# Kernel optimization log

Hardware: AMD Instinct MI355X
Metric: run time of the kernel (lower is better)

Reference implementation:

```python
import jax, jax.numpy as jnp
import numpy as np

B = 4096      # batch size per view (init arg bs)
D = 256       # embedding dim
TEMP = 0.5    # init arg temp
EPS = 1e-8    # torch CosineSimilarity eps


def setup_inputs() -> dict:
    key = jax.random.key(0)
    k1, k2 = jax.random.split(key)
    return {
        "emb1": jax.random.normal(k1, (B, D), dtype=jnp.float32),
        "emb2": jax.random.normal(k2, (B, D), dtype=jnp.float32),
    }


def reference(emb1, emb2):
    # z: (2B, D)
    z = jnp.concatenate([emb1, emb2], axis=0)
    n = 2 * B
    # Cosine similarity as normalize + GEMM (same math as broadcast CosineSimilarity):
    # sim[i,j] = (z_i . z_j) / max(||z_i||*||z_j||, eps), then / temp
    norms = jnp.linalg.norm(z, axis=-1)                       # (2B,)
    denom = jnp.maximum(norms[:, None] * norms[None, :], EPS)  # (2B,2B)
    sim = (z @ z.T) / denom / TEMP                             # (2B,2B)

    idx = jnp.arange(n)
    # positives: diag(sim, +B) then diag(sim, -B) == sim[i, (i+B) mod 2B]
    pos = sim[idx, (idx + B) % n]                              # (2B,)

    # logits row i = [pos_i, negatives_i] = all sim[i,:] except the diagonal.
    # cross-entropy with label 0: loss_i = -pos_i + logsumexp(row without diag)
    diag_mask = idx[:, None] == idx[None, :]
    sim_masked = jnp.where(diag_mask, -jnp.inf, sim)
    lse = jax.nn.logsumexp(sim_masked, axis=-1)                # (2B,)

    loss = jnp.sum(lse - pos) / n   # CrossEntropyLoss(reduction='sum') / 2B
    return loss
```

## Files before the change

kernel.cpp:

```cpp
#include <hip/hip_runtime.h>
#include <hip/hip_bf16.h>


constexpr int kN  = 8192;
constexpr int kD  = 256;
constexpr int kBH = 4096;
constexpr int kChunks  = 32;
constexpr int kColsPer = kN / kChunks;
constexpr float kInvTemp = 2.0f;
constexpr float kInvTempLog2e = 2.8853900817779268f;

typedef __attribute__((ext_vector_type(8))) short bf16x8;
typedef __attribute__((ext_vector_type(4))) float f32x4;

__device__ __forceinline__ unsigned short f2bf(float f) {
  union { float f; unsigned u; } x;
  x.f = f;
  unsigned u = x.u;
  return (unsigned short)((u + 0x7FFFu + ((u >> 16) & 1u)) >> 16);
}

__global__ void k_normalize(const float* __restrict__ e1,
                            const float* __restrict__ e2,
                            unsigned short* __restrict__ zn,
                            float* __restrict__ accum ) {
  if (blockIdx.x < 16) {
    float4 z4 = {0.f, 0.f, 0.f, 0.f};
    *reinterpret_cast<float4*>(accum + blockIdx.x * 1024 + threadIdx.x * 4) = z4;
  }
  const int wave = threadIdx.x >> 6;
  const int lane = threadIdx.x & 63;
  const int row  = blockIdx.x * 4 + wave;
  const float* src = (row < kBH) ? (e1 + (size_t)row * kD)
                                 : (e2 + (size_t)(row - kBH) * kD);
  float4 v = *reinterpret_cast<const float4*>(src + lane * 4);
  float ssq = v.x * v.x + v.y * v.y + v.z * v.z + v.w * v.w;
#pragma unroll
  for (int m = 1; m < 64; m <<= 1) ssq += __shfl_xor(ssq, m);
  const float inv = 1.0f / sqrtf(ssq);
  ushort4 o;
  o.x = f2bf(v.x * inv);
  o.y = f2bf(v.y * inv);
  o.z = f2bf(v.z * inv);
  o.w = f2bf(v.w * inv);
  const int g  = row >> 4;
  const int rr = row & 15;
  const size_t dst = (size_t)g * 4096 + (lane >> 3) * 512 +
                     ((lane >> 1) & 3) * 128 + rr * 8 + (lane & 1) * 4;
  *reinterpret_cast<ushort4*>(zn + dst) = o;
}

__global__ __launch_bounds__(256, 4)
void k_simlse(const unsigned short* __restrict__ zn,
              float* __restrict__ s_sum,
              float* __restrict__ pos_sum) {
  const int bid = blockIdx.x;
  const int rt  = bid >> 5;
  const int ch  = bid & 31;
  const int wave = threadIdx.x >> 6;
  const int lane = threadIdx.x & 63;
  const int l15 = lane & 15;
  const int lhi = lane >> 4;
  const int rowBase = rt * 128 + wave * 32;
  const int colBase = ch * kColsPer;

  bf16x8 a[2][8];
#pragma unroll
  for (int s = 0; s < 2; ++s) {
    const unsigned short* ap =
        zn + (size_t)((rowBase >> 4) + s) * 4096 + lane * 8;
#pragma unroll
    for (int ks = 0; ks < 8; ++ks)
      a[s][ks] = *reinterpret_cast<const bf16x8*>(ap + ks * 512);
  }

  float sacc[2][4] = {{0.f, 0.f, 0.f, 0.f}, {0.f, 0.f, 0.f, 0.f}};
  float pacc[2][4] = {{0.f, 0.f, 0.f, 0.f}, {0.f, 0.f, 0.f, 0.f}};

  for (int ct = 0; ct < kColsPer / 16; ++ct) {
    const int cb = colBase + ct * 16;
    const unsigned short* bp = zn + (size_t)(cb >> 4) * 4096 + lane * 8;
    bf16x8 b[8];
#pragma unroll
    for (int ks = 0; ks < 8; ++ks)
      b[ks] = *reinterpret_cast<const bf16x8*>(bp + ks * 512);

    f32x4 acc0 = {0.f, 0.f, 0.f, 0.f};
    f32x4 acc1 = {0.f, 0.f, 0.f, 0.f};
#pragma unroll
    for (int ks = 0; ks < 8; ++ks) {
      acc0 = __builtin_amdgcn_mfma_f32_16x16x32_bf16(a[0][ks], b[ks], acc0, 0, 0, 0);
      acc1 = __builtin_amdgcn_mfma_f32_16x16x32_bf16(a[1][ks], b[ks], acc1, 0, 0, 0);
    }

    const int c = cb + l15;
#pragma unroll
    for (int s = 0; s < 2; ++s) {
      const f32x4 acc = s ? acc1 : acc0;
      const int rbase16 = rowBase + s * 16;
      const bool diagT = (cb == rbase16);
      const bool posT  = (cb == ((rbase16 + kBH) & (kN - 1)));
      if (!diagT && !posT) {
#pragma unroll
        for (int j = 0; j < 4; ++j)
          sacc[s][j] += exp2f(acc[j] * kInvTempLog2e);
      } else {
#pragma unroll
        for (int j = 0; j < 4; ++j) {
          const int row = rbase16 + lhi * 4 + j;
          const float v = acc[j] * kInvTemp;
          float p = exp2f(acc[j] * kInvTempLog2e);
          if (diagT && c == row) p = 0.0f;
          if (posT && c == ((row + kBH) & (kN - 1))) pacc[s][j] += v;
          sacc[s][j] += p;
        }
      }
    }
  }

#pragma unroll
  for (int s = 0; s < 2; ++s) {
    const int rbase16 = rowBase + s * 16;
    const int pc = (rbase16 + kBH) & (kN - 1);
    const bool hasPos = (pc >= colBase) && (pc < colBase + kColsPer);
#pragma unroll
    for (int j = 0; j < 4; ++j) {
      float sv = sacc[s][j];
      float pv = pacc[s][j];
#pragma unroll
      for (int m = 1; m < 16; m <<= 1) {
        sv += __shfl_xor(sv, m);
        pv += __shfl_xor(pv, m);
      }
      if (l15 == 0) {
        const int row = rbase16 + lhi * 4 + j;
        atomicAdd(&s_sum[row], sv);
        if (hasPos) atomicAdd(&pos_sum[row], pv);
      }
    }
  }
}

__global__ void k_final(const float* __restrict__ s_sum,
                        const float* __restrict__ pos_sum,
                        float* __restrict__ out) {
  __shared__ float red[16];
  float acc = 0.0f;
  for (int r = threadIdx.x; r < kN; r += 1024)
    acc += logf(s_sum[r]) - pos_sum[r];
#pragma unroll
  for (int m = 1; m < 64; m <<= 1) acc += __shfl_xor(acc, m);
  const int wave = threadIdx.x >> 6;
  const int lane = threadIdx.x & 63;
  if (lane == 0) red[wave] = acc;
  __syncthreads();
  if (threadIdx.x == 0) {
    float t = 0.0f;
#pragma unroll
    for (int w = 0; w < 16; ++w) t += red[w];
    out[0] = t / (float)kN;
  }
}

extern "C" void kernel_launch(void* const* d_in, const int* in_sizes, int n_in,
                              void* d_out, int out_size, void* d_ws, size_t ws_size,
                              hipStream_t stream) {
  const float* e1 = (const float*)d_in[0];
  const float* e2 = (const float*)d_in[1];
  float* out = (float*)d_out;

  unsigned short* zn = (unsigned short*)d_ws;
  float* s_sum   = (float*)((char*)d_ws + (size_t)kN * kD * 2);
  float* pos_sum = s_sum + kN;

  hipLaunchKernelGGL(k_normalize, dim3(kN / 4), dim3(256), 0, stream,
                     e1, e2, zn, s_sum);
  hipLaunchKernelGGL(k_simlse, dim3(64 * kChunks), dim3(256), 0, stream,
                     zn, s_sum, pos_sum);
  hipLaunchKernelGGL(k_final, dim3(1), dim3(1024), 0, stream,
                     s_sum, pos_sum, out);
}
```

Before: 65.83 us.

## Fold temperature scale into normalization and double-buffer B tile loads

Normalized rows are scaled by sqrt(2*log2e) so the MFMA output feeds exp2 directly with no per-element multiply, and the positive term is recovered by multiplying by ln2. The column loop becomes a ping-pong pipeline that prefetches the next 16-column B fragment while MFMAs run on the current one. Occupancy is relaxed to 3 waves per SIMD to make room for the extra registers. Scaling before bf16 rounding slightly changes the rounding, and the last prefetch reads a wrapped, unused tile.

```diff
diff --git a/kernel.cpp b/kernel.cpp
--- a/kernel.cpp
+++ b/kernel.cpp
@@ -7,8 +7,8 @@
 constexpr int kBH = 4096;
 constexpr int kChunks  = 32;
 constexpr int kColsPer = kN / kChunks;
-constexpr float kInvTemp = 2.0f;
-constexpr float kInvTempLog2e = 2.8853900817779268f;
+constexpr float kSqrtScale = 1.6986436f;
+constexpr float kLn2 = 0.6931471805599453f;
 
 typedef __attribute__((ext_vector_type(8))) short bf16x8;
 typedef __attribute__((ext_vector_type(4))) float f32x4;
@@ -37,12 +37,12 @@
   float ssq = v.x * v.x + v.y * v.y + v.z * v.z + v.w * v.w;
 #pragma unroll
   for (int m = 1; m < 64; m <<= 1) ssq += __shfl_xor(ssq, m);
-  const float inv = 1.0f / sqrtf(ssq);
+  const float invs = kSqrtScale / sqrtf(ssq);
   ushort4 o;
-  o.x = f2bf(v.x * inv);
-  o.y = f2bf(v.y * inv);
-  o.z = f2bf(v.z * inv);
-  o.w = f2bf(v.w * inv);
+  o.x = f2bf(v.x * invs);
+  o.y = f2bf(v.y * invs);
+  o.z = f2bf(v.z * invs);
+  o.w = f2bf(v.w * invs);
   const int g  = row >> 4;
   const int rr = row & 15;
   const size_t dst = (size_t)g * 4096 + (lane >> 3) * 512 +
@@ -50,7 +50,7 @@
   *reinterpret_cast<ushort4*>(zn + dst) = o;
 }
 
-__global__ __launch_bounds__(256, 4)
+__global__ __launch_bounds__(256, 3)
 void k_simlse(const unsigned short* __restrict__ zn,
               float* __restrict__ s_sum,
               float* __restrict__ pos_sum) {
@@ -64,35 +64,37 @@
   const int rowBase = rt * 128 + wave * 32;
   const int colBase = ch * kColsPer;
 
-  bf16x8 a[2][8];
+  bf16x8 a0[8], a1[8];
+  {
+    const unsigned short* ap0 = zn + (size_t)(rowBase >> 4) * 4096 + lane * 8;
 #pragma unroll
-  for (int s = 0; s < 2; ++s) {
-    const unsigned short* ap =
-        zn + (size_t)((rowBase >> 4) + s) * 4096 + lane * 8;
-#pragma unroll
-    for (int ks = 0; ks < 8; ++ks)
-      a[s][ks] = *reinterpret_cast<const bf16x8*>(ap + ks * 512);
+    for (int ks = 0; ks < 8; ++ks) {
+      a0[ks] = *reinterpret_cast<const bf16x8*>(ap0 + ks * 512);
+      a1[ks] = *reinterpret_cast<const bf16x8*>(ap0 + 4096 + ks * 512);
+    }
   }
 
   float sacc[2][4] = {{0.f, 0.f, 0.f, 0.f}, {0.f, 0.f, 0.f, 0.f}};
   float pacc[2][4] = {{0.f, 0.f, 0.f, 0.f}, {0.f, 0.f, 0.f, 0.f}};
 
-  for (int ct = 0; ct < kColsPer / 16; ++ct) {
-    const int cb = colBase + ct * 16;
-    const unsigned short* bp = zn + (size_t)(cb >> 4) * 4096 + lane * 8;
-    bf16x8 b[8];
+  bf16x8 bA[8], bB[8];
+
+  auto loadB = [&](bf16x8* b, int cb) {
+    const unsigned short* bp =
+        zn + (size_t)((cb & (kN - 1)) >> 4) * 4096 + lane * 8;
 #pragma unroll
     for (int ks = 0; ks < 8; ++ks)
       b[ks] = *reinterpret_cast<const bf16x8*>(bp + ks * 512);
+  };
 
+  auto computeT = [&](const bf16x8* b, int cb) {
     f32x4 acc0 = {0.f, 0.f, 0.f, 0.f};
     f32x4 acc1 = {0.f, 0.f, 0.f, 0.f};
 #pragma unroll
     for (int ks = 0; ks < 8; ++ks) {
-      acc0 = __builtin_amdgcn_mfma_f32_16x16x32_bf16(a[0][ks], b[ks], acc0, 0, 0, 0);
-      acc1 = __builtin_amdgcn_mfma_f32_16x16x32_bf16(a[1][ks], b[ks], acc1, 0, 0, 0);
+      acc0 = __builtin_amdgcn_mfma_f32_16x16x32_bf16(a0[ks], b[ks], acc0, 0, 0, 0);
+      acc1 = __builtin_amdgcn_mfma_f32_16x16x32_bf16(a1[ks], b[ks], acc1, 0, 0, 0);
     }
-
     const int c = cb + l15;
 #pragma unroll
     for (int s = 0; s < 2; ++s) {
@@ -103,19 +105,30 @@
       if (!diagT && !posT) {
 #pragma unroll
         for (int j = 0; j < 4; ++j)
-          sacc[s][j] += exp2f(acc[j] * kInvTempLog2e);
+          sacc[s][j] += exp2f(acc[j]);
       } else {
 #pragma unroll
         for (int j = 0; j < 4; ++j) {
           const int row = rbase16 + lhi * 4 + j;
-          const float v = acc[j] * kInvTemp;
-          float p = exp2f(acc[j] * kInvTempLog2e);
+          const float v = acc[j] * kLn2;
+          float p = exp2f(acc[j]);
           if (diagT && c == row) p = 0.0f;
           if (posT && c == ((row + kBH) & (kN - 1))) pacc[s][j] += v;
           sacc[s][j] += p;
         }
       }
     }
+  };
+
+  int cb = colBase;
+  loadB(bA, cb);
+#pragma unroll 1
+  for (int it = 0; it < kColsPer / 32; ++it) {
+    loadB(bB, cb + 16);
+    computeT(bA, cb);
+    loadB(bA, cb + 32);
+    computeT(bB, cb + 16);
+    cb += 32;
   }
 
 #pragma unroll
```

After: 62.82 us. 4.6% less time.

## Stage shared B tiles in LDS with double buffering, enlarge row tile, fold scale

Applied to the files above, without the earlier changes.

Each block now covers 256 rows (64 per wave, 4 MFMA row groups) and pulls each 16-column B tile once into LDS through async global_load_lds, double-buffered. Before, every wave loaded its own copy from global memory. The 1/temp*log2e factor is split as a sqrt and folded into the normalized embeddings, so the exp needs no multiply. The aim is to cut redundant global/L2 traffic for B and improve MFMA reuse. The cost is more registers for the A fragments (occupancy hint drops to 2), two barriers per tile, and a prefetch that wraps around to a dummy tile at the end.

```diff
diff --git a/kernel.cpp b/kernel.cpp
--- a/kernel.cpp
+++ b/kernel.cpp
@@ -7,8 +7,9 @@
 constexpr int kBH = 4096;
 constexpr int kChunks  = 32;
 constexpr int kColsPer = kN / kChunks;
-constexpr float kInvTemp = 2.0f;
-constexpr float kInvTempLog2e = 2.8853900817779268f;
+constexpr int kNT = kColsPer / 16;
+constexpr float kSqrtScale = 1.6986436f;
+constexpr float kLn2 = 0.6931471805599453f;
 
 typedef __attribute__((ext_vector_type(8))) short bf16x8;
 typedef __attribute__((ext_vector_type(4))) float f32x4;
@@ -18,6 +19,12 @@
   x.f = f;
   unsigned u = x.u;
   return (unsigned short)((u + 0x7FFFu + ((u >> 16) & 1u)) >> 16);
+}
+
+__device__ __forceinline__ void gload_lds16(const short* g, short* l) {
+  __builtin_amdgcn_global_load_lds(
+      (const __attribute__((address_space(1))) void*)g,
+      (__attribute__((address_space(3))) void*)l, 16, 0, 0);
 }
 
 __global__ void k_normalize(const float* __restrict__ e1,
@@ -37,12 +44,12 @@
   float ssq = v.x * v.x + v.y * v.y + v.z * v.z + v.w * v.w;
 #pragma unroll
   for (int m = 1; m < 64; m <<= 1) ssq += __shfl_xor(ssq, m);
-  const float inv = 1.0f / sqrtf(ssq);
+  const float invs = kSqrtScale / sqrtf(ssq);
   ushort4 o;
-  o.x = f2bf(v.x * inv);
-  o.y = f2bf(v.y * inv);
-  o.z = f2bf(v.z * inv);
-  o.w = f2bf(v.w * inv);
+  o.x = f2bf(v.x * invs);
+  o.y = f2bf(v.y * invs);
+  o.z = f2bf(v.z * invs);
+  o.w = f2bf(v.w * invs);
   const int g  = row >> 4;
   const int rr = row & 15;
   const size_t dst = (size_t)g * 4096 + (lane >> 3) * 512 +
@@ -50,10 +57,12 @@
   *reinterpret_cast<ushort4*>(zn + dst) = o;
 }
 
-__global__ __launch_bounds__(256, 4)
+__global__ __launch_bounds__(256, 2)
 void k_simlse(const unsigned short* __restrict__ zn,
               float* __restrict__ s_sum,
               float* __restrict__ pos_sum) {
+  __shared__ __align__(16) short ldsB[2][4096];
+
   const int bid = blockIdx.x;
   const int rt  = bid >> 5;
   const int ch  = bid & 31;
@@ -61,12 +70,21 @@
   const int lane = threadIdx.x & 63;
   const int l15 = lane & 15;
   const int lhi = lane >> 4;
-  const int rowBase = rt * 128 + wave * 32;
+  const int rowBase = rt * 256 + wave * 64;
   const int colBase = ch * kColsPer;
-
-  bf16x8 a[2][8];
-#pragma unroll
-  for (int s = 0; s < 2; ++s) {
+  const int grpBase = colBase >> 4;
+
+  auto stage = [&](int buf, int tile) {
+    const short* src = (const short*)zn + (size_t)(grpBase + tile) * 4096 +
+                       wave * 1024;
+    short* dst = &ldsB[buf][wave * 1024];
+    gload_lds16(src + lane * 8, dst);
+    gload_lds16(src + 512 + lane * 8, dst + 512);
+  };
+
+  bf16x8 a[4][8];
+#pragma unroll
+  for (int s = 0; s < 4; ++s) {
     const unsigned short* ap =
         zn + (size_t)((rowBase >> 4) + s) * 4096 + lane * 8;
 #pragma unroll
@@ -74,52 +92,68 @@
       a[s][ks] = *reinterpret_cast<const bf16x8*>(ap + ks * 512);
   }
 
-  float sacc[2][4] = {{0.f, 0.f, 0.f, 0.f}, {0.f, 0.f, 0.f, 0.f}};
-  float pacc[2][4] = {{0.f, 0.f, 0.f, 0.f}, {0.f, 0.f, 0.f, 0.f}};
-
-  for (int ct = 0; ct < kColsPer / 16; ++ct) {
-    const int cb = colBase + ct * 16;
-    const unsigned short* bp = zn + (size_t)(cb >> 4) * 4096 + lane * 8;
+  float sacc[4][4];
+  float pacc[4][4];
+#pragma unroll
+  for (int s = 0; s < 4; ++s)
+#pragma unroll
+    for (int j = 0; j < 4; ++j) { sacc[s][j] = 0.f; pacc[s][j] = 0.f; }
+
+  stage(0, 0);
+
+#pragma unroll 1
+  for (int t = 0; t < kNT; ++t) {
+    stage((t + 1) & 1, (t + 1) & (kNT - 1));
+    asm volatile("s_waitcnt vmcnt(2)" ::: "memory");
+    __builtin_amdgcn_s_barrier();
+
+    const short* bt = &ldsB[t & 1][0];
     bf16x8 b[8];
 #pragma unroll
     for (int ks = 0; ks < 8; ++ks)
-      b[ks] = *reinterpret_cast<const bf16x8*>(bp + ks * 512);
-
-    f32x4 acc0 = {0.f, 0.f, 0.f, 0.f};
-    f32x4 acc1 = {0.f, 0.f, 0.f, 0.f};
+      b[ks] = *reinterpret_cast<const bf16x8*>(bt + ks * 512 + lane * 8);
+
+    f32x4 acc[4];
+#pragma unroll
+    for (int s = 0; s < 4; ++s) acc[s] = {0.f, 0.f, 0.f, 0.f};
 #pragma unroll
     for (int ks = 0; ks < 8; ++ks) {
-      acc0 = __builtin_amdgcn_mfma_f32_16x16x32_bf16(a[0][ks], b[ks], acc0, 0, 0, 0);
-      acc1 = __builtin_amdgcn_mfma_f32_16x16x32_bf16(a[1][ks], b[ks], acc1, 0, 0, 0);
+      const bf16x8 bk = b[ks];
+#pragma unroll
+      for (int s = 0; s < 4; ++s)
+        acc[s] = __builtin_amdgcn_mfma_f32_16x16x32_bf16(a[s][ks], bk, acc[s], 0, 0, 0);
     }
 
-    const int c = cb + l15;
-#pragma unroll
-    for (int s = 0; s < 2; ++s) {
-      const f32x4 acc = s ? acc1 : acc0;
+    const int cb = colBase + t * 16;
+    const int c  = cb + l15;
+#pragma unroll
+    for (int s = 0; s < 4; ++s) {
       const int rbase16 = rowBase + s * 16;
       const bool diagT = (cb == rbase16);
       const bool posT  = (cb == ((rbase16 + kBH) & (kN - 1)));
       if (!diagT && !posT) {
 #pragma unroll
         for (int j = 0; j < 4; ++j)
-          sacc[s][j] += exp2f(acc[j] * kInvTempLog2e);
+          sacc[s][j] += exp2f(acc[s][j]);
       } else {
 #pragma unroll
         for (int j = 0; j < 4; ++j) {
           const int row = rbase16 + lhi * 4 + j;
-          const float v = acc[j] * kInvTemp;
-          float p = exp2f(acc[j] * kInvTempLog2e);
+          const float v = acc[s][j] * kLn2;
+          float p = exp2f(acc[s][j]);
           if (diagT && c == row) p = 0.0f;
           if (posT && c == ((row + kBH) & (kN - 1))) pacc[s][j] += v;
           sacc[s][j] += p;
         }
       }
     }
-  }
-
-#pragma unroll
-  for (int s = 0; s < 2; ++s) {
+
+    __builtin_amdgcn_s_barrier();
+    asm volatile("" ::: "memory");
+  }
+
+#pragma unroll
+  for (int s = 0; s < 4; ++s) {
     const int rbase16 = rowBase + s * 16;
     const int pc = (rbase16 + kBH) & (kN - 1);
     const bool hasPos = (pc >= colBase) && (pc < colBase + kColsPer);
@@ -175,7 +209,7 @@
 
   hipLaunchKernelGGL(k_normalize, dim3(kN / 4), dim3(256), 0, stream,
                      e1, e2, zn, s_sum);
-  hipLaunchKernelGGL(k_simlse, dim3(64 * kChunks), dim3(256), 0, stream,
+  hipLaunchKernelGGL(k_simlse, dim3(32 * kChunks), dim3(256), 0, stream,
                      zn, s_sum, pos_sum);
   hipLaunchKernelGGL(k_final, dim3(1), dim3(1024), 0, stream,
                      s_sum, pos_sum, out);
```

New measurement: 62.35 us. -5.3%, faster.
